# Kernel optimization log

Hardware: AMD Instinct MI355X
Metric: run time of the kernel (lower is better)

## Reference

```python
import jax, jax.numpy as jnp
import numpy as np

EPS = 0.05
MAX_ITER = 100


def setup_inputs() -> dict:
    key = jax.random.key(0)
    k1, k2, k3 = jax.random.split(key, 3)
    B, D, N = 16, 64, 1024
    x = jax.random.normal(k1, (B, D, N), dtype=jnp.float32)
    y = jax.random.normal(k2, (B, D, N), dtype=jnp.float32)
    C = jax.random.uniform(k3, (B, N, N), dtype=jnp.float32)
    return {"x": x, "y": y, "C": C}


def reference(x, y, C):
    # x: (B, D, N), y: (B, D, N) -- only last dim (number of points) is used.
    B = C.shape[0]
    N = x.shape[-1]
    cons = jnp.full((B, N, 1), 1.0 / N, dtype=jnp.float32)  # (B, N, 1)
    U = jnp.exp(-C / EPS)          # (B, N, N)
    V = jnp.swapaxes(U, 1, 2)      # U^T, (B, N, N)

    def body(carry, _):
        mu, _ = carry
        nu = cons / jnp.matmul(U, mu)   # (B, N, 1)
        mu_new = cons / jnp.matmul(V, nu)
        return (mu_new, nu), None

    (mu, nu), _ = jax.lax.scan(body, (cons, cons), None, length=MAX_ITER)
    # T = mu * U * nu^T, broadcast over rows/cols
    T = mu * U * jnp.swapaxes(nu, 1, 2)  # (B, N, N)
    return T
```

## Files before the change

kernel.cpp:

```cpp
#include <hip/hip_runtime.h>
#include <math.h>

#define B_    16
#define N_    1024
#define G_    16
#define ITERS 100

#define MUDEN_OFF   8192
#define MUDEN_BYTES (4 * B_ * N_ * 4)
#define NUG_OFF     (MUDEN_OFF + MUDEN_BYTES)
#define ZERO_BYTES  NUG_OFF

__device__ __forceinline__ float fast_div(float num, float den) {
    float r = __builtin_amdgcn_rcpf(den);
    r = r * (2.0f - den * r);
    return num * r;
}

__device__ __forceinline__ float wave_sum64(float x) {
#define DPP_ADD(ctrl)                                                   \
    x += __int_as_float(__builtin_amdgcn_update_dpp(                    \
            0, __float_as_int(x), ctrl, 0xf, 0xf, false));
    DPP_ADD(0x111)
    DPP_ADD(0x112)
    DPP_ADD(0x114)
    DPP_ADD(0x118)
    DPP_ADD(0x142)
    DPP_ADD(0x143)
#undef DPP_ADD
    return __int_as_float(__builtin_amdgcn_readlane(__float_as_int(x), 63));
}

__global__ __launch_bounds__(1024, 4)
void sinkhorn_kernel(const float* __restrict__ C, float* __restrict__ out,
                     float* __restrict__ mu_den, float* __restrict__ nug,
                     unsigned int* __restrict__ cnt)
{
    __shared__ float part[16 * 1024];
    __shared__ float mu_s[N_];

    const int tid = threadIdx.x;
    const int w   = tid >> 6;
    const int l   = tid & 63;
    const int bid = blockIdx.x;
    const int xx = bid & 7, ss = bid >> 3;
    const int b = xx + ((ss >> 4) << 3);
    const int g = ss & 15;
    const int row0 = 64 * g + 4 * w;
    const float cons = 1.0f / 1024.0f;

    float u[4][16];
    {
        const float* Cb = C + (size_t)b * N_ * N_ + (size_t)row0 * N_;
        #pragma unroll
        for (int rr = 0; rr < 4; ++rr)
            #pragma unroll
            for (int ch = 0; ch < 4; ++ch) {
                float4 cv = *(const float4*)(Cb + (size_t)rr * N_ + 4 * l + 256 * ch);
                u[rr][4*ch+0] = expf(-20.0f * cv.x);
                u[rr][4*ch+1] = expf(-20.0f * cv.y);
                u[rr][4*ch+2] = expf(-20.0f * cv.z);
                u[rr][4*ch+3] = expf(-20.0f * cv.w);
            }
    }

    mu_s[tid] = cons;
    __syncthreads();

    for (int it = 0; it < ITERS; ++it) {
        float a0 = 0.f, a1 = 0.f, a2 = 0.f, a3 = 0.f;
        #pragma unroll
        for (int ch = 0; ch < 4; ++ch) {
            float4 mv = *(const float4*)&mu_s[4 * l + 256 * ch];
            a0 += u[0][4*ch+0]*mv.x + u[0][4*ch+1]*mv.y + u[0][4*ch+2]*mv.z + u[0][4*ch+3]*mv.w;
            a1 += u[1][4*ch+0]*mv.x + u[1][4*ch+1]*mv.y + u[1][4*ch+2]*mv.z + u[1][4*ch+3]*mv.w;
            a2 += u[2][4*ch+0]*mv.x + u[2][4*ch+1]*mv.y + u[2][4*ch+2]*mv.z + u[2][4*ch+3]*mv.w;
            a3 += u[3][4*ch+0]*mv.x + u[3][4*ch+1]*mv.y + u[3][4*ch+2]*mv.z + u[3][4*ch+3]*mv.w;
        }
        a0 = wave_sum64(a0);
        a1 = wave_sum64(a1);
        a2 = wave_sum64(a2);
        a3 = wave_sum64(a3);
        float nu0 = fast_div(cons, a0);
        float nu1 = fast_div(cons, a1);
        float nu2 = fast_div(cons, a2);
        float nu3 = fast_div(cons, a3);

        if (it == ITERS - 1 && l < 4) {
            float nv = (l == 0) ? nu0 : (l == 1) ? nu1 : (l == 2) ? nu2 : nu3;
            __hip_atomic_store(&nug[b * N_ + row0 + l], nv,
                               __ATOMIC_RELAXED, __HIP_MEMORY_SCOPE_AGENT);
        }

        #pragma unroll
        for (int ch = 0; ch < 4; ++ch) {
            float4 p;
            p.x = u[0][4*ch+0]*nu0 + u[1][4*ch+0]*nu1 + u[2][4*ch+0]*nu2 + u[3][4*ch+0]*nu3;
            p.y = u[0][4*ch+1]*nu0 + u[1][4*ch+1]*nu1 + u[2][4*ch+1]*nu2 + u[3][4*ch+1]*nu3;
            p.z = u[0][4*ch+2]*nu0 + u[1][4*ch+2]*nu1 + u[2][4*ch+2]*nu2 + u[3][4*ch+2]*nu3;
            p.w = u[0][4*ch+3]*nu0 + u[1][4*ch+3]*nu1 + u[2][4*ch+3]*nu2 + u[3][4*ch+3]*nu3;
            *(float4*)&part[w * 1024 + 4 * l + 256 * ch] = p;
        }
        __syncthreads();

        const int buf = it & 3;
        {
            float ssum = 0.f;
            #pragma unroll
            for (int w2 = 0; w2 < 16; ++w2)
                ssum += part[w2 * 1024 + tid];
            unsafeAtomicAdd(&mu_den[((size_t)buf * B_ + b) * N_ + tid], ssum);
        }

        __syncthreads();
        if (tid == 0) {
            unsigned int* c = &cnt[b * ITERS + it];
            __hip_atomic_fetch_add(c, 1u, __ATOMIC_RELAXED, __HIP_MEMORY_SCOPE_AGENT);
            while (__hip_atomic_load(c, __ATOMIC_RELAXED, __HIP_MEMORY_SCOPE_AGENT) < G_)
                __builtin_amdgcn_s_sleep(1);
        }
        __syncthreads();

        {
            float den = __hip_atomic_load(&mu_den[((size_t)buf * B_ + b) * N_ + tid],
                                          __ATOMIC_RELAXED, __HIP_MEMORY_SCOPE_AGENT);
            mu_s[tid] = fast_div(cons, den);
        }
        if (tid < 64)
            __hip_atomic_store(&mu_den[((size_t)((it + 2) & 3) * B_ + b) * N_ + 64 * g + tid],
                               0.0f, __ATOMIC_RELAXED, __HIP_MEMORY_SCOPE_AGENT);
        __syncthreads();
    }

    float mu_i[4];
    #pragma unroll
    for (int rr = 0; rr < 4; ++rr)
        mu_i[rr] = mu_s[row0 + rr];

    float* ob = out + (size_t)b * N_ * N_ + (size_t)row0 * N_;
    #pragma unroll
    for (int ch = 0; ch < 4; ++ch) {
        const int cbase = b * N_ + 4 * l + 256 * ch;
        float4 nuv;
        nuv.x = __hip_atomic_load(&nug[cbase + 0], __ATOMIC_RELAXED, __HIP_MEMORY_SCOPE_AGENT);
        nuv.y = __hip_atomic_load(&nug[cbase + 1], __ATOMIC_RELAXED, __HIP_MEMORY_SCOPE_AGENT);
        nuv.z = __hip_atomic_load(&nug[cbase + 2], __ATOMIC_RELAXED, __HIP_MEMORY_SCOPE_AGENT);
        nuv.w = __hip_atomic_load(&nug[cbase + 3], __ATOMIC_RELAXED, __HIP_MEMORY_SCOPE_AGENT);
        #pragma unroll
        for (int rr = 0; rr < 4; ++rr) {
            float4 t;
            t.x = mu_i[rr] * u[rr][4*ch+0] * nuv.x;
            t.y = mu_i[rr] * u[rr][4*ch+1] * nuv.y;
            t.z = mu_i[rr] * u[rr][4*ch+2] * nuv.z;
            t.w = mu_i[rr] * u[rr][4*ch+3] * nuv.w;
            *(float4*)(ob + (size_t)rr * N_ + 4 * l + 256 * ch) = t;
        }
    }
}

extern "C" void kernel_launch(void* const* d_in, const int* in_sizes, int n_in,
                              void* d_out, int out_size, void* d_ws, size_t ws_size,
                              hipStream_t stream) {
    const float* C = (const float*)d_in[2];
    float* out = (float*)d_out;

    unsigned char* ws = (unsigned char*)d_ws;
    unsigned int* cnt = (unsigned int*)ws;
    float* mu_den = (float*)(ws + MUDEN_OFF);
    float* nug    = (float*)(ws + NUG_OFF);

    hipMemsetAsync(ws, 0, ZERO_BYTES, stream);
    hipLaunchKernelGGL(sinkhorn_kernel, dim3(256), dim3(1024), 0, stream,
                       C, out, mu_den, nug, cnt);
}
```

Measured before the change: 398.8 us.

## Halve block size and give each wave eight rows of U

Each block now runs 8 waves of 512 threads instead of 16, and each wave keeps 8 rows of exp(-C/eps) in registers instead of 4. This halves the shared-memory partial buffer and the number of per-column partial sums reduced per iteration, and each shared mu load is reused across more rows. In exchange it uses twice the registers per thread (128 floats for U) and has fewer waves to hide latency, with each thread now handling two columns in the reduction and the mu update.

```diff
diff --git a/kernel.cpp b/kernel.cpp
--- a/kernel.cpp
+++ b/kernel.cpp
@@ -4,6 +4,7 @@
 #define B_    16
 #define N_    1024
 #define G_    16
+#define NW    8
 #define ITERS 100
 
 #define MUDEN_OFF   8192
@@ -31,12 +32,12 @@
     return __int_as_float(__builtin_amdgcn_readlane(__float_as_int(x), 63));
 }
 
-__global__ __launch_bounds__(1024, 4)
+__global__ __launch_bounds__(512, 2)
 void sinkhorn_kernel(const float* __restrict__ C, float* __restrict__ out,
                      float* __restrict__ mu_den, float* __restrict__ nug,
                      unsigned int* __restrict__ cnt)
 {
-    __shared__ float part[16 * 1024];
+    __shared__ float part[NW * 1024];
     __shared__ float mu_s[N_];
 
     const int tid = threadIdx.x;
@@ -46,14 +47,14 @@
     const int xx = bid & 7, ss = bid >> 3;
     const int b = xx + ((ss >> 4) << 3);
     const int g = ss & 15;
-    const int row0 = 64 * g + 4 * w;
+    const int row0 = 64 * g + 8 * w;
     const float cons = 1.0f / 1024.0f;
 
-    float u[4][16];
+    float u[8][16];
     {
         const float* Cb = C + (size_t)b * N_ * N_ + (size_t)row0 * N_;
         #pragma unroll
-        for (int rr = 0; rr < 4; ++rr)
+        for (int rr = 0; rr < 8; ++rr)
             #pragma unroll
             for (int ch = 0; ch < 4; ++ch) {
                 float4 cv = *(const float4*)(Cb + (size_t)rr * N_ + 4 * l + 256 * ch);
@@ -64,30 +65,34 @@
             }
     }
 
-    mu_s[tid] = cons;
+    mu_s[tid]       = cons;
+    mu_s[tid + 512] = cons;
     __syncthreads();
 
     for (int it = 0; it < ITERS; ++it) {
         float a0 = 0.f, a1 = 0.f, a2 = 0.f, a3 = 0.f;
+        float a4 = 0.f, a5 = 0.f, a6 = 0.f, a7 = 0.f;
         #pragma unroll
         for (int ch = 0; ch < 4; ++ch) {
             float4 mv = *(const float4*)&mu_s[4 * l + 256 * ch];
-            a0 += u[0][4*ch+0]*mv.x + u[0][4*ch+1]*mv.y + u[0][4*ch+2]*mv.z + u[0][4*ch+3]*mv.w;
-            a1 += u[1][4*ch+0]*mv.x + u[1][4*ch+1]*mv.y + u[1][4*ch+2]*mv.z + u[1][4*ch+3]*mv.w;
-            a2 += u[2][4*ch+0]*mv.x + u[2][4*ch+1]*mv.y + u[2][4*ch+2]*mv.z + u[2][4*ch+3]*mv.w;
-            a3 += u[3][4*ch+0]*mv.x + u[3][4*ch+1]*mv.y + u[3][4*ch+2]*mv.z + u[3][4*ch+3]*mv.w;
+#define PHA(rr) a##rr += u[rr][4*ch+0]*mv.x + u[rr][4*ch+1]*mv.y \
+                       + u[rr][4*ch+2]*mv.z + u[rr][4*ch+3]*mv.w;
+            PHA(0) PHA(1) PHA(2) PHA(3) PHA(4) PHA(5) PHA(6) PHA(7)
+#undef PHA
         }
-        a0 = wave_sum64(a0);
-        a1 = wave_sum64(a1);
-        a2 = wave_sum64(a2);
-        a3 = wave_sum64(a3);
-        float nu0 = fast_div(cons, a0);
-        float nu1 = fast_div(cons, a1);
-        float nu2 = fast_div(cons, a2);
-        float nu3 = fast_div(cons, a3);
+        a0 = wave_sum64(a0); a1 = wave_sum64(a1);
+        a2 = wave_sum64(a2); a3 = wave_sum64(a3);
+        a4 = wave_sum64(a4); a5 = wave_sum64(a5);
+        a6 = wave_sum64(a6); a7 = wave_sum64(a7);
+        float nu0 = fast_div(cons, a0), nu1 = fast_div(cons, a1);
+        float nu2 = fast_div(cons, a2), nu3 = fast_div(cons, a3);
+        float nu4 = fast_div(cons, a4), nu5 = fast_div(cons, a5);
+        float nu6 = fast_div(cons, a6), nu7 = fast_div(cons, a7);
 
-        if (it == ITERS - 1 && l < 4) {
-            float nv = (l == 0) ? nu0 : (l == 1) ? nu1 : (l == 2) ? nu2 : nu3;
+        if (it == ITERS - 1 && l < 8) {
+            float nv = (l == 0) ? nu0 : (l == 1) ? nu1 : (l == 2) ? nu2 :
+                       (l == 3) ? nu3 : (l == 4) ? nu4 : (l == 5) ? nu5 :
+                       (l == 6) ? nu6 : nu7;
             __hip_atomic_store(&nug[b * N_ + row0 + l], nv,
                                __ATOMIC_RELAXED, __HIP_MEMORY_SCOPE_AGENT);
         }
@@ -95,21 +100,26 @@
         #pragma unroll
         for (int ch = 0; ch < 4; ++ch) {
             float4 p;
-            p.x = u[0][4*ch+0]*nu0 + u[1][4*ch+0]*nu1 + u[2][4*ch+0]*nu2 + u[3][4*ch+0]*nu3;
-            p.y = u[0][4*ch+1]*nu0 + u[1][4*ch+1]*nu1 + u[2][4*ch+1]*nu2 + u[3][4*ch+1]*nu3;
-            p.z = u[0][4*ch+2]*nu0 + u[1][4*ch+2]*nu1 + u[2][4*ch+2]*nu2 + u[3][4*ch+2]*nu3;
-            p.w = u[0][4*ch+3]*nu0 + u[1][4*ch+3]*nu1 + u[2][4*ch+3]*nu2 + u[3][4*ch+3]*nu3;
+#define PB(s) (u[0][4*ch+s]*nu0 + u[1][4*ch+s]*nu1 + u[2][4*ch+s]*nu2 + \
+               u[3][4*ch+s]*nu3 + u[4][4*ch+s]*nu4 + u[5][4*ch+s]*nu5 + \
+               u[6][4*ch+s]*nu6 + u[7][4*ch+s]*nu7)
+            p.x = PB(0); p.y = PB(1); p.z = PB(2); p.w = PB(3);
+#undef PB
             *(float4*)&part[w * 1024 + 4 * l + 256 * ch] = p;
         }
         __syncthreads();
 
         const int buf = it & 3;
         {
-            float ssum = 0.f;
+            float s0 = 0.f, s1 = 0.f;
             #pragma unroll
-            for (int w2 = 0; w2 < 16; ++w2)
-                ssum += part[w2 * 1024 + tid];
-            unsafeAtomicAdd(&mu_den[((size_t)buf * B_ + b) * N_ + tid], ssum);
+            for (int w2 = 0; w2 < NW; ++w2) {
+                s0 += part[w2 * 1024 + tid];
+                s1 += part[w2 * 1024 + tid + 512];
+            }
+            float* md = &mu_den[((size_t)buf * B_ + b) * N_];
+            unsafeAtomicAdd(md + tid,       s0);
+            unsafeAtomicAdd(md + tid + 512, s1);
         }
 
         __syncthreads();
@@ -122,9 +132,13 @@
         __syncthreads();
 
         {
-            float den = __hip_atomic_load(&mu_den[((size_t)buf * B_ + b) * N_ + tid],
-                                          __ATOMIC_RELAXED, __HIP_MEMORY_SCOPE_AGENT);
-            mu_s[tid] = fast_div(cons, den);
+            const float* mdb = &mu_den[((size_t)buf * B_ + b) * N_];
+            float den0 = __hip_atomic_load(mdb + tid,
+                                           __ATOMIC_RELAXED, __HIP_MEMORY_SCOPE_AGENT);
+            float den1 = __hip_atomic_load(mdb + tid + 512,
+                                           __ATOMIC_RELAXED, __HIP_MEMORY_SCOPE_AGENT);
+            mu_s[tid]       = fast_div(cons, den0);
+            mu_s[tid + 512] = fast_div(cons, den1);
         }
         if (tid < 64)
             __hip_atomic_store(&mu_den[((size_t)((it + 2) & 3) * B_ + b) * N_ + 64 * g + tid],
@@ -132,9 +146,9 @@
         __syncthreads();
     }
 
-    float mu_i[4];
+    float mu_i[8];
     #pragma unroll
-    for (int rr = 0; rr < 4; ++rr)
+    for (int rr = 0; rr < 8; ++rr)
         mu_i[rr] = mu_s[row0 + rr];
 
     float* ob = out + (size_t)b * N_ * N_ + (size_t)row0 * N_;
@@ -147,7 +161,7 @@
         nuv.z = __hip_atomic_load(&nug[cbase + 2], __ATOMIC_RELAXED, __HIP_MEMORY_SCOPE_AGENT);
         nuv.w = __hip_atomic_load(&nug[cbase + 3], __ATOMIC_RELAXED, __HIP_MEMORY_SCOPE_AGENT);
         #pragma unroll
-        for (int rr = 0; rr < 4; ++rr) {
+        for (int rr = 0; rr < 8; ++rr) {
             float4 t;
             t.x = mu_i[rr] * u[rr][4*ch+0] * nuv.x;
             t.y = mu_i[rr] * u[rr][4*ch+1] * nuv.y;
@@ -170,6 +184,6 @@
     float* nug    = (float*)(ws + NUG_OFF);
 
     hipMemsetAsync(ws, 0, ZERO_BYTES, stream);
-    hipLaunchKernelGGL(sinkhorn_kernel, dim3(256), dim3(1024), 0, stream,
+    hipLaunchKernelGGL(sinkhorn_kernel, dim3(256), dim3(512), 0, stream,
                        C, out, mu_den, nug, cnt);
 }
```

Result: faster. 377.4 us (-5.4%).
